# Kernel tuning notes

Hardware: AMD Instinct MI355X
Metric: run time of the kernel (lower is better)

The kernel has to match this reference:

```python
import jax, jax.numpy as jnp
import numpy as np

NITER = 20  # clus_num_iters (faiss Kmeans niter)


def _kmeans_labels(X, init_idx, niter):
    """Lloyd's k-means on X [N,d] with centroids initialized at X[init_idx]; returns labels [N]."""
    def assign(cent):
        d2 = (cent * cent).sum(-1)[None, :] - 2.0 * (X @ cent.T)  # [N, C]
        return jnp.argmin(d2, axis=1)

    def step(cent, _):
        labels = assign(cent)
        C = cent.shape[0]
        sums = jax.ops.segment_sum(X, labels, num_segments=C)              # [C, d]
        counts = jax.ops.segment_sum(jnp.ones((X.shape[0],), X.dtype), labels, num_segments=C)
        new = jnp.where(counts[:, None] > 0, sums / jnp.maximum(counts, 1.0)[:, None], cent)
        return new, None

    cent0 = X[init_idx]
    cent, _ = jax.lax.scan(step, cent0, None, length=niter)
    return assign(cent)


def setup_inputs() -> dict:
    key = jax.random.key(0)
    k1, k2, k3, k4 = jax.random.split(key, 4)
    N, D, E, K, C = 8192, 256, 131072, 5, 64

    def l2norm(x):
        return x / jnp.linalg.norm(x, axis=-1, keepdims=True)

    # AFGRL passes F.normalize(student/teacher) into Neighbor
    student = l2norm(jax.random.normal(k1, (N, D), dtype=jnp.float32))
    teacher = l2norm(jax.random.normal(k2, (N, D), dtype=jnp.float32))
    edge_index = jax.random.randint(k3, (2, E), 0, N)          # sparse adj COO indices
    kmeans_init_idx = jax.random.randint(k4, (K, C), 0, N)     # per-seed centroid init
    return {
        "student": student,
        "teacher": teacher,
        "edge_index": edge_index,
        "kmeans_init_idx": kmeans_init_idx,
        "top_k": 8,
    }


def reference(student, teacher, edge_index, kmeans_init_idx, top_k):
    n = student.shape[0]
    idx = jnp.arange(n)

    # similarity with +10 on the diagonal (forces self as top-1 neighbor)
    sim = (student @ teacher.T).at[idx, idx].add(10.0)          # [n, n]
    D_knn, I_knn = jax.lax.top_k(sim, top_k)                    # [n, k], sorted desc

    # locality: knn edges that are also present in adj (sparse elementwise product)
    codes_adj = jnp.sort(edge_index[0] * n + edge_index[1])     # [E]
    codes_knn = (idx[:, None] * n + I_knn).ravel()              # [n*k]
    pos = jnp.clip(jnp.searchsorted(codes_adj, codes_knn), 0, codes_adj.shape[0] - 1)
    in_adj = (codes_adj[pos] == codes_knn).reshape(n, top_k)    # [n, k] bool

    # globality: knn edges whose endpoints share a cluster in ANY of the kmeans runs
    labels = jax.vmap(lambda ii: _kmeans_labels(teacher, ii, NITER))(kmeans_init_idx)  # [K, n]
    close = (labels[:, :, None] == labels[:, I_knn]).any(axis=0)  # [n, k] bool

    # pos_ = locality + globality ; coalesced indices == union of masked knn edges
    pos_mask = in_adj | close
    return I_knn, pos_mask, D_knn
```

## Files before the change

### kernel.cpp

```cpp
#include <hip/hip_runtime.h>
#include <hip/hip_bf16.h>
#include <math.h>

#define NN 8192
#define DD 256
#define KSEED 5
#define CC 64
#define TK 8
#define NITERS 20
#define CSPLIT 8
#define BM 128
#define BN 64
#define UB 32
#define NCAND 24

typedef __attribute__((ext_vector_type(8))) short short8v;
typedef __attribute__((ext_vector_type(4))) float f32x4;

#define MFMA(a, b, c) __builtin_amdgcn_mfma_f32_16x16x32_bf16(a, b, c, 0, 0, 0)

__device__ __forceinline__ bool kbetter(float v1, int i1, float v2, int i2) {
    return (v1 > v2) || ((v1 == v2) && (i1 < i2));
}

__device__ __forceinline__ unsigned short f2bf(float x) {
    unsigned u = __float_as_uint(x);
    unsigned r = 0x7fffu + ((u >> 16) & 1u);
    return (unsigned short)((u + r) >> 16);
}
__device__ __forceinline__ float bf2f(unsigned short h) {
    return __uint_as_float(((unsigned)h) << 16);
}

__global__ __launch_bounds__(256) void transpose_k(const float* __restrict__ in,
                                                   float* __restrict__ out) {
    __shared__ float t[32][33];
    int bx = blockIdx.x * 32;
    int by = blockIdx.y * 32;
    int x = threadIdx.x;
    int y = threadIdx.y;
#pragma unroll
    for (int i = 0; i < 32; i += 8)
        t[y + i][x] = in[(size_t)(bx + y + i) * DD + by + x];
    __syncthreads();
#pragma unroll
    for (int i = 0; i < 32; i += 8)
        out[(size_t)(by + y + i) * NN + bx + x] = t[x][y + i];
}

__global__ __launch_bounds__(256) void adj_k(const int* __restrict__ e0,
                                             const int* __restrict__ e1,
                                             unsigned int* __restrict__ bm, int E) {
    int t = blockIdx.x * 256 + threadIdx.x;
    if (t < E) {
        unsigned code = (unsigned)e0[t] * NN + (unsigned)e1[t];
        atomicOr(&bm[code >> 5], 1u << (code & 31));
    }
}

__global__ __launch_bounds__(256) void conv_k(const float* __restrict__ src,
                                              short* __restrict__ hi,
                                              short* __restrict__ lo) {
    int slot = blockIdx.x * 256 + threadIdx.x;
    int l = slot & 63;
    int TS = slot >> 6;
    int S = TS & 7;
    int T = TS >> 3;
    int row = T * 16 + (l & 15);
    int k0 = S * 32 + (l >> 4) * 8;
    const float* p = src + (size_t)row * DD + k0;
    short8v h8, l8;
#pragma unroll
    for (int j = 0; j < 8; j++) {
        float x = p[j];
        unsigned short hb = f2bf(x);
        unsigned short lb = f2bf(x - bf2f(hb));
        h8[j] = (short)hb;
        l8[j] = (short)lb;
    }
    *(short8v*)(hi + (size_t)slot * 8) = h8;
    *(short8v*)(lo + (size_t)slot * 8) = l8;
}

__global__ __launch_bounds__(256) void kinit_k(const float* __restrict__ teacher,
                                               const int* __restrict__ initIdx,
                                               float* __restrict__ centT,
                                               float* __restrict__ cnorm) {
    int c = blockIdx.x, s = blockIdx.y;
    int t = threadIdx.x;
    int src = initIdx[s * CC + c];
    float v = teacher[(size_t)src * DD + t];
    centT[((size_t)s * DD + t) * CC + c] = v;
    __shared__ float red[256];
    red[t] = v * v;
    __syncthreads();
    for (int w = 128; w > 0; w >>= 1) {
        if (t < w) red[t] += red[t + w];
        __syncthreads();
    }
    if (t == 0) cnorm[s * CC + c] = red[0];
}

__global__ __launch_bounds__(256) void kassign_k(const float* __restrict__ tT,
                                                 const float* __restrict__ centT,
                                                 const float* __restrict__ cnorm,
                                                 int* __restrict__ labels) {
    __shared__ float Xs[64 * 64];
    __shared__ float Cs[64 * 64];
    const int s = blockIdx.y;
    const int pB = blockIdx.x * 64;
    const int tid = threadIdx.x;
    const int tx = tid & 15;
    const int ty = tid >> 4;
    float acc[4][4];
#pragma unroll
    for (int a = 0; a < 4; a++)
#pragma unroll
        for (int b = 0; b < 4; b++) acc[a][b] = 0.f;

#pragma unroll 1
    for (int kt = 0; kt < DD; kt += 64) {
        __syncthreads();
#pragma unroll
        for (int m = 0; m < 4; m++) {
            int u = m * 256 + tid;
            int kk = u >> 4;
            int p4 = (u & 15) << 2;
            *(float4*)&Xs[kk * 64 + p4] =
                *(const float4*)&tT[(size_t)(kt + kk) * NN + pB + p4];
            *(float4*)&Cs[kk * 64 + p4] =
                *(const float4*)&centT[((size_t)s * DD + kt + kk) * CC + p4];
        }
        __syncthreads();
#pragma unroll 8
        for (int kk = 0; kk < 64; kk++) {
            float4 x4 = *(float4*)&Xs[kk * 64 + 4 * ty];
            float4 c4 = *(float4*)&Cs[kk * 64 + 4 * tx];
            float xr[4] = {x4.x, x4.y, x4.z, x4.w};
            float cr[4] = {c4.x, c4.y, c4.z, c4.w};
#pragma unroll
            for (int a = 0; a < 4; a++)
#pragma unroll
                for (int b = 0; b < 4; b++) acc[a][b] = fmaf(xr[a], cr[b], acc[a][b]);
        }
    }
    __syncthreads();
    float* red = Cs;
    float cn[4];
#pragma unroll
    for (int b = 0; b < 4; b++) cn[b] = cnorm[s * CC + 4 * tx + b];
#pragma unroll
    for (int a = 0; a < 4; a++) {
        float bv = INFINITY;
        int bc = 0;
#pragma unroll
        for (int b = 0; b < 4; b++) {
            float d = fmaf(-2.f, acc[a][b], cn[b]);
            if (d < bv) { bv = d; bc = 4 * tx + b; }
        }
        int p = 4 * ty + a;
        red[(p * 16 + tx) * 2] = bv;
        ((int*)red)[(p * 16 + tx) * 2 + 1] = bc;
    }
    __syncthreads();
    if (tid < 64) {
        float bv = INFINITY;
        int bc = 0;
        for (int t2 = 0; t2 < 16; t2++) {
            float v = red[(tid * 16 + t2) * 2];
            int c = ((int*)red)[(tid * 16 + t2) * 2 + 1];
            if (v < bv) { bv = v; bc = c; }
        }
        labels[(size_t)s * NN + pB + tid] = bc;
    }
}

__global__ __launch_bounds__(256) void kupd12_k(const float* __restrict__ teacher,
                                                const int* __restrict__ labels,
                                                float* __restrict__ centT,
                                                float* __restrict__ cnorm) {
    const int c = blockIdx.x;
    const int s = blockIdx.y;
    const int t = threadIdx.x;
    __shared__ int list[NN];
    __shared__ float stage[UB * DD];
    __shared__ int scan_s[256];
    __shared__ float red[256];
    __shared__ int total_s;

    const int* labS = labels + (size_t)s * NN;

    int my = 0;
#pragma unroll
    for (int j = 0; j < 32; j++) my += (labS[t * 32 + j] == c);
    scan_s[t] = my;
    __syncthreads();
    for (int off = 1; off < 256; off <<= 1) {
        int v = (t >= off) ? scan_s[t - off] : 0;
        __syncthreads();
        scan_s[t] += v;
        __syncthreads();
    }
    const int base = scan_s[t] - my;
    if (t == 255) total_s = scan_s[255];
    int pos = base;
#pragma unroll
    for (int j = 0; j < 32; j++) {
        int p = t * 32 + j;
        if (labS[p] == c) list[pos++] = p;
    }
    __syncthreads();
    const int total = total_s;

    float sum = 0.f, part = 0.f;
    int curb = 0;
    for (int g0 = 0; g0 < total; g0 += UB) {
        const int gn = (total - g0 < UB) ? (total - g0) : UB;
        __syncthreads();
        for (int u = t; u < gn * (DD / 4); u += 256) {
            int j = u >> 6;
            int col4 = (u & 63) << 2;
            *(float4*)&stage[j * DD + col4] =
                *(const float4*)&teacher[(size_t)list[g0 + j] * DD + col4];
        }
        __syncthreads();
        for (int j = 0; j < gn; j++) {
            int p = list[g0 + j];
            int b = p >> 8;
            while (curb < b) { sum += part; part = 0.f; curb++; }
            part += stage[j * DD + t];
        }
    }
    while (curb < 32) { sum += part; part = 0.f; curb++; }

    float old = centT[((size_t)s * DD + t) * CC + c];
    float nv = (total > 0) ? (sum / (float)total) : old;
    centT[((size_t)s * DD + t) * CC + c] = nv;
    red[t] = nv * nv;
    __syncthreads();
    for (int w = 128; w > 0; w >>= 1) {
        if (t < w) red[t] += red[t + w];
        __syncthreads();
    }
    if (t == 0) cnorm[s * CC + c] = red[0];
}

__global__ __launch_bounds__(256) void topk_gemm_k(const short* __restrict__ shi,
                                                   const short* __restrict__ slo,
                                                   const short* __restrict__ thi,
                                                   const short* __restrict__ tlo,
                                                   float* __restrict__ pv,
                                                   int* __restrict__ pi) {
    __shared__ float smem[BM * BN];

    const int split = blockIdx.x;
    const int rowB = blockIdx.y * BM;
    const int tid = threadIdx.x;
    const int w = tid >> 6;
    const int lane = tid & 63;
    const int rl = lane & 15;
    const int lh = lane >> 4;
    const int sr = tid >> 1;
    const int sh = tid & 1;

    float tv[TK];
    int ti[TK];
#pragma unroll
    for (int q = 0; q < TK; q++) { tv[q] = -INFINITY; ti[q] = 0x7fffffff; }

    const int colBase = split * (NN / CSPLIT);
    const int TA0 = (rowB >> 4) + 2 * w;

#pragma unroll 1
    for (int ct = 0; ct < (NN / CSPLIT) / BN; ct++) {
        const int colB = colBase + ct * BN;
        const int U0 = colB >> 4;
        f32x4 acc[2][4];
#pragma unroll
        for (int rt = 0; rt < 2; rt++)
#pragma unroll
            for (int ut = 0; ut < 4; ut++) acc[rt][ut] = (f32x4){0.f, 0.f, 0.f, 0.f};

#pragma unroll 1
        for (int S = 0; S < 8; S++) {
            const size_t a0off = ((size_t)(TA0 * 8 + S) * 64 + lane) * 8;
            const size_t a1off = ((size_t)((TA0 + 1) * 8 + S) * 64 + lane) * 8;
            short8v ah0 = *(const short8v*)(shi + a0off);
            short8v ah1 = *(const short8v*)(shi + a1off);
            short8v al0 = *(const short8v*)(slo + a0off);
            short8v al1 = *(const short8v*)(slo + a1off);
#pragma unroll
            for (int ut = 0; ut < 4; ut++) {
                const size_t boff = ((size_t)((U0 + ut) * 8 + S) * 64 + lane) * 8;
                short8v bh = *(const short8v*)(thi + boff);
                short8v bl = *(const short8v*)(tlo + boff);
                acc[0][ut] = MFMA(ah0, bh, acc[0][ut]);
                acc[0][ut] = MFMA(ah0, bl, acc[0][ut]);
                acc[0][ut] = MFMA(al0, bh, acc[0][ut]);
                acc[1][ut] = MFMA(ah1, bh, acc[1][ut]);
                acc[1][ut] = MFMA(ah1, bl, acc[1][ut]);
                acc[1][ut] = MFMA(al1, bh, acc[1][ut]);
            }
        }
        __syncthreads();
#pragma unroll
        for (int rt = 0; rt < 2; rt++)
#pragma unroll
            for (int ut = 0; ut < 4; ut++)
#pragma unroll
                for (int reg = 0; reg < 4; reg++) {
                    int r_loc = 32 * w + 16 * rt + 4 * lh + reg;
                    int cl = 16 * ut + rl;
                    float v = acc[rt][ut][reg];
                    if (rowB + r_loc == colB + cl) v += 10.f;
                    smem[r_loc * 64 + (cl ^ (r_loc & 31))] = v;
                }
        __syncthreads();
#pragma unroll 4
        for (int c = 0; c < 32; c++) {
            int cb2 = sh * 32 + c;
            float v = smem[sr * 64 + (cb2 ^ (sr & 31))];
            int gcol = colB + cb2;
            if (kbetter(v, gcol, tv[TK - 1], ti[TK - 1])) {
                tv[TK - 1] = v;
                ti[TK - 1] = gcol;
#pragma unroll
                for (int q = TK - 1; q > 0; --q) {
                    if (kbetter(tv[q], ti[q], tv[q - 1], ti[q - 1])) {
                        float t1 = tv[q]; tv[q] = tv[q - 1]; tv[q - 1] = t1;
                        int t2 = ti[q]; ti[q] = ti[q - 1]; ti[q - 1] = t2;
                    }
                }
            }
        }
    }
    int row = rowB + sr;
#pragma unroll
    for (int q = 0; q < TK; q++) {
        pv[((size_t)row * CSPLIT + split) * 16 + sh * 8 + q] = tv[q];
        pi[((size_t)row * CSPLIT + split) * 16 + sh * 8 + q] = ti[q];
    }
}

__global__ __launch_bounds__(256) void topk_merge_k(const float* __restrict__ pv,
                                                    const int* __restrict__ pi,
                                                    int* __restrict__ cand) {
    const int tid = threadIdx.x;
    const int wid = tid >> 6;
    const int lane = tid & 63;
    const int row = blockIdx.x * 4 + wid;
    const size_t base = (size_t)row * (CSPLIT * 16);

    float v0 = pv[base + lane];
    float v1 = pv[base + 64 + lane];
    unsigned i0 = (unsigned)pi[base + lane];
    unsigned i1 = (unsigned)pi[base + 64 + lane];
    unsigned s0 = __float_as_uint(v0);
    unsigned s1 = __float_as_uint(v1);
    unsigned m0 = (s0 & 0x80000000u) ? ~s0 : (s0 | 0x80000000u);
    unsigned m1 = (s1 & 0x80000000u) ? ~s1 : (s1 | 0x80000000u);
    unsigned long long k0 = (((unsigned long long)m0) << 32) | (0xFFFFFFFFu - i0);
    unsigned long long k1 = (((unsigned long long)m1) << 32) | (0xFFFFFFFFu - i1);

    for (int o = 0; o < NCAND; o++) {
        unsigned long long m = k0 > k1 ? k0 : k1;
#pragma unroll
        for (int off = 32; off > 0; off >>= 1) {
            unsigned long long other = __shfl_xor(m, off, 64);
            if (other > m) m = other;
        }
        if (lane == 0)
            cand[row * NCAND + o] = (int)(0xFFFFFFFFu - (unsigned)(m & 0xFFFFFFFFu));
        if (k0 == m) k0 = 0;
        if (k1 == m) k1 = 0;
    }
}

__global__ __launch_bounds__(256) void rescore_k(const float* __restrict__ student,
                                                 const float* __restrict__ teacher,
                                                 const int* __restrict__ cand,
                                                 int* __restrict__ iknn,
                                                 float* __restrict__ dknn) {
    __shared__ float srow[4 * DD];
    __shared__ int clist[4 * NCAND];
    __shared__ float cv[4 * NCAND];
    __shared__ int civ[4 * NCAND];
    const int tid = threadIdx.x;
    const int r0 = blockIdx.x * 4;
    *(float4*)&srow[tid * 4] = *(const float4*)&student[(size_t)r0 * DD + tid * 4];
    for (int i = tid; i < 4 * NCAND; i += 256) clist[i] = cand[r0 * NCAND + i];
    __syncthreads();
    const int w = tid >> 6;
    const int lane = tid & 63;
    const int r = r0 + w;
    if (lane < NCAND) {
        int c = clist[w * NCAND + lane];
        const float* tr = teacher + (size_t)c * DD;
        const float* sw = srow + w * DD;
        float acc = 0.f;
#pragma unroll 8
        for (int k = 0; k < DD; k += 4) {
            float4 t4 = *(const float4*)&tr[k];
            acc = fmaf(sw[k], t4.x, acc);
            acc = fmaf(sw[k + 1], t4.y, acc);
            acc = fmaf(sw[k + 2], t4.z, acc);
            acc = fmaf(sw[k + 3], t4.w, acc);
        }
        if (c == r) acc += 10.f;
        cv[w * NCAND + lane] = acc;
        civ[w * NCAND + lane] = c;
    }
    __syncthreads();
    if (lane == 0) {
        unsigned used = 0;
        for (int o = 0; o < TK; o++) {
            float bv = -INFINITY;
            int bi = 0x7fffffff;
            int bsel = -1;
            for (int m = 0; m < NCAND; m++) {
                if ((used >> m) & 1u) continue;
                float v = cv[w * NCAND + m];
                int ix = civ[w * NCAND + m];
                if (bsel < 0 || kbetter(v, ix, bv, bi)) { bv = v; bi = ix; bsel = m; }
            }
            used |= 1u << bsel;
            iknn[r * TK + o] = bi;
            dknn[r * TK + o] = bv;
        }
    }
}

__global__ __launch_bounds__(256) void out_k(const int* __restrict__ iknn,
                                             const float* __restrict__ dknn,
                                             const unsigned int* __restrict__ bm,
                                             const int* __restrict__ labels,
                                             float* __restrict__ out) {
    int t = blockIdx.x * 256 + threadIdx.x;
    int row = t >> 3;
    int ki = iknn[t];
    unsigned code = (unsigned)row * NN + (unsigned)ki;
    bool adj = (bm[code >> 5] >> (code & 31)) & 1u;
    bool close = false;
#pragma unroll
    for (int s = 0; s < KSEED; s++)
        close |= (labels[s * NN + row] == labels[s * NN + ki]);
    out[t] = (float)ki;
    out[NN * TK + t] = (adj || close) ? 1.0f : 0.0f;
    out[2 * NN * TK + t] = dknn[t];
}

extern "C" void kernel_launch(void* const* d_in, const int* in_sizes, int n_in,
                              void* d_out, int out_size, void* d_ws, size_t ws_size,
                              hipStream_t stream) {
    (void)n_in; (void)out_size; (void)ws_size;
    const float* student = (const float*)d_in[0];
    const float* teacher = (const float*)d_in[1];
    const int* edge = (const int*)d_in[2];
    const int* initIdx = (const int*)d_in[3];
    const int E = in_sizes[2] / 2;

    char* ws = (char*)d_ws;
    size_t off = 0;
    auto alloc = [&](size_t bytes) -> char* {
        char* p = ws + off;
        off += (bytes + 255) & ~(size_t)255;
        return p;
    };
    unsigned int* bm = (unsigned int*)alloc((size_t)NN * NN / 8);
    float* tT = (float*)alloc((size_t)NN * DD * 4);
    short* shi = (short*)alloc((size_t)NN * DD * 2);
    short* slo = (short*)alloc((size_t)NN * DD * 2);
    short* thi = (short*)alloc((size_t)NN * DD * 2);
    short* tlo = (short*)alloc((size_t)NN * DD * 2);
    float* centT = (float*)alloc((size_t)KSEED * DD * CC * 4);
    float* cnorm = (float*)alloc((size_t)KSEED * CC * 4);
    int* labels = (int*)alloc((size_t)KSEED * NN * 4);
    float* pv = (float*)alloc((size_t)NN * CSPLIT * 16 * 4);
    int* pi = (int*)alloc((size_t)NN * CSPLIT * 16 * 4);
    int* cand = (int*)alloc((size_t)NN * NCAND * 4);
    int* iknn = (int*)alloc((size_t)NN * TK * 4);
    float* dknn = (float*)alloc((size_t)NN * TK * 4);
    float* out = (float*)d_out;

    hipMemsetAsync(bm, 0, (size_t)NN * NN / 8, stream);
    adj_k<<<dim3((E + 255) / 256), 256, 0, stream>>>(edge, edge + E, bm, E);
    transpose_k<<<dim3(NN / 32, DD / 32), dim3(32, 8), 0, stream>>>(teacher, tT);
    conv_k<<<dim3(NN * DD / 8 / 256), 256, 0, stream>>>(student, shi, slo);
    conv_k<<<dim3(NN * DD / 8 / 256), 256, 0, stream>>>(teacher, thi, tlo);

    kinit_k<<<dim3(CC, KSEED), 256, 0, stream>>>(teacher, initIdx, centT, cnorm);
    for (int it = 0; it < NITERS; ++it) {
        kassign_k<<<dim3(NN / 64, KSEED), 256, 0, stream>>>(tT, centT, cnorm, labels);
        kupd12_k<<<dim3(CC, KSEED), 256, 0, stream>>>(teacher, labels, centT, cnorm);
    }
    kassign_k<<<dim3(NN / 64, KSEED), 256, 0, stream>>>(tT, centT, cnorm, labels);

    topk_gemm_k<<<dim3(CSPLIT, NN / BM), 256, 0, stream>>>(shi, slo, thi, tlo, pv, pi);
    topk_merge_k<<<dim3(NN / 4), 256, 0, stream>>>(pv, pi, cand);
    rescore_k<<<dim3(NN / 4), 256, 0, stream>>>(student, teacher, cand, iknn, dknn);
    out_k<<<dim3(NN * TK / 256), 256, 0, stream>>>(iknn, dknn, bm, labels, out);
}
```

Measured before the change: 1.839 ms.

## Move k-means assignment GEMM to split-bf16 MFMA with fp32 winner rescoring

The k-means assignment kernel now computes point-centroid dot products with bf16x3 MFMA instructions. It reuses the teacher hi/lo fragments already built for the top-k GEMM, and the update kernels write centroid hi/lo fragments directly, so the teacher transpose and the fp32 scalar-FMA tiling go away. Each lane keeps its best centroid, recomputes that distance exactly in fp32 from row-major centroids, and reduces across lanes with shuffles. The risk is that split-bf16 approximation picks a different argmin than the reference when distances are nearly tied.

```diff
diff --git a/kernel.cpp b/kernel.cpp
--- a/kernel.cpp
+++ b/kernel.cpp
@@ -32,20 +32,8 @@
     return __uint_as_float(((unsigned)h) << 16);
 }
 
-__global__ __launch_bounds__(256) void transpose_k(const float* __restrict__ in,
-                                                   float* __restrict__ out) {
-    __shared__ float t[32][33];
-    int bx = blockIdx.x * 32;
-    int by = blockIdx.y * 32;
-    int x = threadIdx.x;
-    int y = threadIdx.y;
-#pragma unroll
-    for (int i = 0; i < 32; i += 8)
-        t[y + i][x] = in[(size_t)(bx + y + i) * DD + by + x];
-    __syncthreads();
-#pragma unroll
-    for (int i = 0; i < 32; i += 8)
-        out[(size_t)(by + y + i) * NN + bx + x] = t[x][y + i];
+__device__ __forceinline__ size_t fragidx(int row, int k) {
+    return (((size_t)(row >> 4) * 8 + (k >> 5)) * 64 + ((k >> 3) & 3) * 16 + (row & 15)) * 8 + (k & 7);
 }
 
 __global__ __launch_bounds__(256) void adj_k(const int* __restrict__ e0,
@@ -84,13 +72,20 @@
 
 __global__ __launch_bounds__(256) void kinit_k(const float* __restrict__ teacher,
                                                const int* __restrict__ initIdx,
-                                               float* __restrict__ centT,
-                                               float* __restrict__ cnorm) {
+                                               float* __restrict__ centR,
+                                               float* __restrict__ cnorm,
+                                               short* __restrict__ chi,
+                                               short* __restrict__ clo) {
     int c = blockIdx.x, s = blockIdx.y;
     int t = threadIdx.x;
     int src = initIdx[s * CC + c];
     float v = teacher[(size_t)src * DD + t];
-    centT[((size_t)s * DD + t) * CC + c] = v;
+    centR[((size_t)s * CC + c) * DD + t] = v;
+    unsigned short hb = f2bf(v);
+    unsigned short lb = f2bf(v - bf2f(hb));
+    size_t idx = (size_t)s * 16384 + fragidx(c, t);
+    chi[idx] = (short)hb;
+    clo[idx] = (short)lb;
     __shared__ float red[256];
     red[t] = v * v;
     __syncthreads();
@@ -101,84 +96,99 @@
     if (t == 0) cnorm[s * CC + c] = red[0];
 }
 
-__global__ __launch_bounds__(256) void kassign_k(const float* __restrict__ tT,
-                                                 const float* __restrict__ centT,
+__global__ __launch_bounds__(256) void kassign_k(const float* __restrict__ teacher,
+                                                 const short* __restrict__ thi,
+                                                 const short* __restrict__ tlo,
+                                                 const short* __restrict__ chi,
+                                                 const short* __restrict__ clo,
+                                                 const float* __restrict__ centR,
                                                  const float* __restrict__ cnorm,
                                                  int* __restrict__ labels) {
-    __shared__ float Xs[64 * 64];
-    __shared__ float Cs[64 * 64];
+    __shared__ float cns[CC];
     const int s = blockIdx.y;
-    const int pB = blockIdx.x * 64;
+    const int pB = blockIdx.x * 256;
     const int tid = threadIdx.x;
-    const int tx = tid & 15;
-    const int ty = tid >> 4;
-    float acc[4][4];
-#pragma unroll
-    for (int a = 0; a < 4; a++)
-#pragma unroll
-        for (int b = 0; b < 4; b++) acc[a][b] = 0.f;
+    const int w = tid >> 6;
+    const int lane = tid & 63;
+    const int rl = lane & 15;
+    const int lh = lane >> 4;
+    if (tid < CC) cns[tid] = cnorm[s * CC + tid];
+    __syncthreads();
+
+    const short* chS = chi + (size_t)s * 16384;
+    const short* clS = clo + (size_t)s * 16384;
+
+    f32x4 acc[4][4];
+#pragma unroll
+    for (int i = 0; i < 4; i++)
+#pragma unroll
+        for (int ct = 0; ct < 4; ct++) acc[i][ct] = (f32x4){0.f, 0.f, 0.f, 0.f};
 
 #pragma unroll 1
-    for (int kt = 0; kt < DD; kt += 64) {
-        __syncthreads();
-#pragma unroll
-        for (int m = 0; m < 4; m++) {
-            int u = m * 256 + tid;
-            int kk = u >> 4;
-            int p4 = (u & 15) << 2;
-            *(float4*)&Xs[kk * 64 + p4] =
-                *(const float4*)&tT[(size_t)(kt + kk) * NN + pB + p4];
-            *(float4*)&Cs[kk * 64 + p4] =
-                *(const float4*)&centT[((size_t)s * DD + kt + kk) * CC + p4];
-        }
-        __syncthreads();
-#pragma unroll 8
-        for (int kk = 0; kk < 64; kk++) {
-            float4 x4 = *(float4*)&Xs[kk * 64 + 4 * ty];
-            float4 c4 = *(float4*)&Cs[kk * 64 + 4 * tx];
-            float xr[4] = {x4.x, x4.y, x4.z, x4.w};
-            float cr[4] = {c4.x, c4.y, c4.z, c4.w};
-#pragma unroll
-            for (int a = 0; a < 4; a++)
-#pragma unroll
-                for (int b = 0; b < 4; b++) acc[a][b] = fmaf(xr[a], cr[b], acc[a][b]);
-        }
-    }
-    __syncthreads();
-    float* red = Cs;
-    float cn[4];
-#pragma unroll
-    for (int b = 0; b < 4; b++) cn[b] = cnorm[s * CC + 4 * tx + b];
-#pragma unroll
-    for (int a = 0; a < 4; a++) {
-        float bv = INFINITY;
+    for (int S = 0; S < 8; S++) {
+        short8v bh[4], bl[4];
+#pragma unroll
+        for (int i = 0; i < 4; i++) {
+            const int U = (pB >> 4) + 4 * w + i;
+            const size_t boff = ((size_t)(U * 8 + S) * 64 + lane) * 8;
+            bh[i] = *(const short8v*)(thi + boff);
+            bl[i] = *(const short8v*)(tlo + boff);
+        }
+#pragma unroll
+        for (int ct = 0; ct < 4; ct++) {
+            const size_t aoff = ((size_t)(ct * 8 + S) * 64 + lane) * 8;
+            short8v ah = *(const short8v*)(chS + aoff);
+            short8v al = *(const short8v*)(clS + aoff);
+#pragma unroll
+            for (int i = 0; i < 4; i++) {
+                acc[i][ct] = MFMA(ah, bh[i], acc[i][ct]);
+                acc[i][ct] = MFMA(ah, bl[i], acc[i][ct]);
+                acc[i][ct] = MFMA(al, bh[i], acc[i][ct]);
+            }
+        }
+    }
+
+#pragma unroll 1
+    for (int i = 0; i < 4; i++) {
+        float bd = INFINITY;
         int bc = 0;
 #pragma unroll
-        for (int b = 0; b < 4; b++) {
-            float d = fmaf(-2.f, acc[a][b], cn[b]);
-            if (d < bv) { bv = d; bc = 4 * tx + b; }
-        }
-        int p = 4 * ty + a;
-        red[(p * 16 + tx) * 2] = bv;
-        ((int*)red)[(p * 16 + tx) * 2 + 1] = bc;
-    }
-    __syncthreads();
-    if (tid < 64) {
-        float bv = INFINITY;
-        int bc = 0;
-        for (int t2 = 0; t2 < 16; t2++) {
-            float v = red[(tid * 16 + t2) * 2];
-            int c = ((int*)red)[(tid * 16 + t2) * 2 + 1];
-            if (v < bv) { bv = v; bc = c; }
-        }
-        labels[(size_t)s * NN + pB + tid] = bc;
+        for (int ct = 0; ct < 4; ct++)
+#pragma unroll
+            for (int reg = 0; reg < 4; reg++) {
+                int c = 16 * ct + 4 * lh + reg;
+                float d = fmaf(-2.f, acc[i][ct][reg], cns[c]);
+                if (d < bd) { bd = d; bc = c; }
+            }
+        const int gp = pB + 16 * (4 * w + i) + rl;
+        const float* tr = teacher + (size_t)gp * DD;
+        const float* cr = centR + ((size_t)s * CC + bc) * DD;
+        float dot = 0.f;
+        for (int k = 0; k < DD; k += 4) {
+            float4 t4 = *(const float4*)&tr[k];
+            float4 c4 = *(const float4*)&cr[k];
+            dot = fmaf(t4.x, c4.x, dot);
+            dot = fmaf(t4.y, c4.y, dot);
+            dot = fmaf(t4.z, c4.z, dot);
+            dot = fmaf(t4.w, c4.w, dot);
+        }
+        float de = fmaf(-2.f, dot, cns[bc]);
+#pragma unroll
+        for (int off = 16; off <= 32; off <<= 1) {
+            float od = __shfl_xor(de, off, 64);
+            int oc = __shfl_xor(bc, off, 64);
+            if (od < de || (od == de && oc < bc)) { de = od; bc = oc; }
+        }
+        if (lh == 0) labels[(size_t)s * NN + gp] = bc;
     }
 }
 
 __global__ __launch_bounds__(256) void kupd12_k(const float* __restrict__ teacher,
                                                 const int* __restrict__ labels,
-                                                float* __restrict__ centT,
-                                                float* __restrict__ cnorm) {
+                                                float* __restrict__ centR,
+                                                float* __restrict__ cnorm,
+                                                short* __restrict__ chi,
+                                                short* __restrict__ clo) {
     const int c = blockIdx.x;
     const int s = blockIdx.y;
     const int t = threadIdx.x;
@@ -233,9 +243,14 @@
     }
     while (curb < 32) { sum += part; part = 0.f; curb++; }
 
-    float old = centT[((size_t)s * DD + t) * CC + c];
+    float old = centR[((size_t)s * CC + c) * DD + t];
     float nv = (total > 0) ? (sum / (float)total) : old;
-    centT[((size_t)s * DD + t) * CC + c] = nv;
+    centR[((size_t)s * CC + c) * DD + t] = nv;
+    unsigned short hb = f2bf(nv);
+    unsigned short lb = f2bf(nv - bf2f(hb));
+    size_t idx = (size_t)s * 16384 + fragidx(c, t);
+    chi[idx] = (short)hb;
+    clo[idx] = (short)lb;
     red[t] = nv * nv;
     __syncthreads();
     for (int w = 128; w > 0; w >>= 1) {
@@ -467,13 +482,14 @@
         return p;
     };
     unsigned int* bm = (unsigned int*)alloc((size_t)NN * NN / 8);
-    float* tT = (float*)alloc((size_t)NN * DD * 4);
     short* shi = (short*)alloc((size_t)NN * DD * 2);
     short* slo = (short*)alloc((size_t)NN * DD * 2);
     short* thi = (short*)alloc((size_t)NN * DD * 2);
     short* tlo = (short*)alloc((size_t)NN * DD * 2);
-    float* centT = (float*)alloc((size_t)KSEED * DD * CC * 4);
+    float* centR = (float*)alloc((size_t)KSEED * CC * DD * 4);
     float* cnorm = (float*)alloc((size_t)KSEED * CC * 4);
+    short* chi = (short*)alloc((size_t)KSEED * 16384 * 2);
+    short* clo = (short*)alloc((size_t)KSEED * 16384 * 2);
     int* labels = (int*)alloc((size_t)KSEED * NN * 4);
     float* pv = (float*)alloc((size_t)NN * CSPLIT * 16 * 4);
     int* pi = (int*)alloc((size_t)NN * CSPLIT * 16 * 4);
@@ -484,16 +500,17 @@
 
     hipMemsetAsync(bm, 0, (size_t)NN * NN / 8, stream);
     adj_k<<<dim3((E + 255) / 256), 256, 0, stream>>>(edge, edge + E, bm, E);
-    transpose_k<<<dim3(NN / 32, DD / 32), dim3(32, 8), 0, stream>>>(teacher, tT);
     conv_k<<<dim3(NN * DD / 8 / 256), 256, 0, stream>>>(student, shi, slo);
     conv_k<<<dim3(NN * DD / 8 / 256), 256, 0, stream>>>(teacher, thi, tlo);
 
-    kinit_k<<<dim3(CC, KSEED), 256, 0, stream>>>(teacher, initIdx, centT, cnorm);
+    kinit_k<<<dim3(CC, KSEED), 256, 0, stream>>>(teacher, initIdx, centR, cnorm, chi, clo);
     for (int it = 0; it < NITERS; ++it) {
-        kassign_k<<<dim3(NN / 64, KSEED), 256, 0, stream>>>(tT, centT, cnorm, labels);
-        kupd12_k<<<dim3(CC, KSEED), 256, 0, stream>>>(teacher, labels, centT, cnorm);
-    }
-    kassign_k<<<dim3(NN / 64, KSEED), 256, 0, stream>>>(tT, centT, cnorm, labels);
+        kassign_k<<<dim3(NN / 256, KSEED), 256, 0, stream>>>(teacher, thi, tlo, chi, clo,
+                                                             centR, cnorm, labels);
+        kupd12_k<<<dim3(CC, KSEED), 256, 0, stream>>>(teacher, labels, centR, cnorm, chi, clo);
+    }
+    kassign_k<<<dim3(NN / 256, KSEED), 256, 0, stream>>>(teacher, thi, tlo, chi, clo,
+                                                         centR, cnorm, labels);
 
     topk_gemm_k<<<dim3(CSPLIT, NN / BM), 256, 0, stream>>>(shi, slo, thi, tlo, pv, pi);
     topk_merge_k<<<dim3(NN / 4), 256, 0, stream>>>(pv, pi, cand);
```

Result: slower. 2.753 ms (+49.7%).
